# Optimization experiments

Hardware: AMD Instinct MI355X
Metric: run time of the kernel (lower is better)

Reference implementation:

```python
import jax, jax.numpy as jnp
import numpy as np

N, D, DOUT = 8192, 128, 128

def setup_inputs() -> dict:
    key = jax.random.key(0)
    k0, k1, k2, k3, k4 = jax.random.split(key, 5)
    return {
        "inputs": jnp.zeros((N, DOUT, 1, 2), jnp.float32),   # output buffer, scatter target
        "adj_pos": jax.random.uniform(k0, (N, N), jnp.float32),
        "adj_neg": jax.random.uniform(k1, (N, N), jnp.float32),
        "h0": jax.random.normal(k2, (N, D), jnp.float32),
        "WB0": jax.random.normal(k3, (DOUT, 2 * D), jnp.float32) * 0.05,
        "WU0": jax.random.normal(k4, (DOUT, 2 * D), jnp.float32) * 0.05,
        "start": 0,
        "end": N,
    }

def reference(inputs, adj_pos, adj_neg, h0, WB0, WU0, start, end):
    # self vectors for the row range [start, end)
    self_vec = h0[start:end]                                   # [n, D]

    def branch(adj, W):
        mask = adj[start:end]                                  # [n, N]
        # masked neighbor aggregation (dense adj matmul) + mean normalization
        agg = (mask @ h0) / jnp.sum(mask, axis=1, keepdims=True)  # [n, D]
        # concat(self-aggregate) -> small matmul (transpose_b=True) -> relu
        feat = jnp.concatenate([agg, self_vec], axis=1)        # [n, 2D]
        return jax.nn.relu(feat @ W.T)                         # [n, DOUT]

    # scatter-assign into the 4-D buffer, slot 0 = balanced, slot 1 = unbalanced
    inputs = inputs.at[start:end, :, 0, 0].set(branch(adj_pos, WB0))
    inputs = inputs.at[start:end, :, 0, 1].set(branch(adj_neg, WU0))
    return inputs
```

## Files before the change

kernel.cpp:

```cpp
#include <hip/hip_runtime.h>
#include <hip/hip_bf16.h>


typedef __bf16 bf16_t;
typedef __attribute__((ext_vector_type(8))) __bf16 bf16x8;
typedef __attribute__((ext_vector_type(4))) float f32x4;

#define KD    8192
#define DD    128
#define NROWS 8192
#define BK    32
#define NSTEP (KD / BK)
#define FLD   136

__device__ __forceinline__ bf16_t to_bf16(float x) { return (bf16_t)x; }

__device__ __forceinline__ bf16x8 cvt8(f32x4 a, f32x4 b) {
    bf16x8 r;
    r[0] = to_bf16(a[0]); r[1] = to_bf16(a[1]); r[2] = to_bf16(a[2]); r[3] = to_bf16(a[3]);
    r[4] = to_bf16(b[0]); r[5] = to_bf16(b[1]); r[6] = to_bf16(b[2]); r[7] = to_bf16(b[3]);
    return r;
}

__global__ void prep_h0T(const float* __restrict__ h0, bf16_t* __restrict__ h0T) {
    __shared__ bf16_t lt[128 * 72];
    const int tid = threadIdx.x;
    const int r0  = blockIdx.x * 64;
#pragma unroll
    for (int i = 0; i < 8; ++i) {
        const int e  = tid + i * 256;
        const int r  = e >> 5;
        const int c4 = e & 31;
        f32x4 v = *(const f32x4*)(h0 + (size_t)(r0 + r) * DD + c4 * 4);
        lt[(c4 * 4 + 0) * 72 + r] = to_bf16(v[0]);
        lt[(c4 * 4 + 1) * 72 + r] = to_bf16(v[1]);
        lt[(c4 * 4 + 2) * 72 + r] = to_bf16(v[2]);
        lt[(c4 * 4 + 3) * 72 + r] = to_bf16(v[3]);
    }
    __syncthreads();
    const int d = tid >> 1, half = tid & 1;
#pragma unroll
    for (int j = 0; j < 4; ++j) {
        bf16x8 v = *(const bf16x8*)(lt + d * 72 + half * 32 + j * 8);
        *(bf16x8*)(h0T + (size_t)d * KD + r0 + half * 32 + j * 8) = v;
    }
}

__global__ __launch_bounds__(256, 1)
void fused_gcn(const float* __restrict__ inputs0,
               const float* __restrict__ adj_pos,
               const float* __restrict__ adj_neg,
               const float* __restrict__ h0,
               const float* __restrict__ WB0,
               const float* __restrict__ WU0,
               const bf16_t* __restrict__ h0T,
               const int* __restrict__ startp,
               const int* __restrict__ endp,
               float* __restrict__ out) {
    __shared__ bf16_t feat[4][16 * FLD];

    const int tid  = threadIdx.x;
    const int wv   = tid >> 6;
    const int lane = tid & 63;
    const int l15  = lane & 15;
    const int quad = lane >> 4;
    const int br   = blockIdx.y;
    const int m0   = (blockIdx.x * 4 + wv) * 16;

    const float* __restrict__ adj  = br ? adj_neg : adj_pos;
    const float* __restrict__ Wmat = br ? WU0 : WB0;

    const float*  ap = adj + (size_t)(m0 + l15) * KD + quad * 8;
    const bf16_t* bp = h0T + (size_t)l15 * KD + quad * 8;

    f32x4 acc[8];
#pragma unroll
    for (int j = 0; j < 8; ++j) acc[j] = (f32x4){0.f, 0.f, 0.f, 0.f};
    float rsum = 0.f;

    f32x4 a0[2], a1[2];
    bf16x8 bfr[2][8];
#pragma unroll
    for (int p = 0; p < 2; ++p) {
        const float* a = ap + p * BK;
        a0[p] = *(const f32x4*)(a);
        a1[p] = *(const f32x4*)(a + 4);
#pragma unroll
        for (int j = 0; j < 8; ++j)
            bfr[p][j] = *(const bf16x8*)(bp + (size_t)j * 16 * KD + p * BK);
    }

#pragma unroll 2
    for (int kt = 0; kt < NSTEP; ++kt) {
        const int p = kt & 1;
        f32x4 va = a0[p], vb = a1[p];
        rsum += va[0] + va[1] + va[2] + va[3] + vb[0] + vb[1] + vb[2] + vb[3];
        bf16x8 afrag = cvt8(va, vb);
        if (kt + 2 < NSTEP) {
            const float* a = ap + (kt + 2) * BK;
            a0[p] = *(const f32x4*)(a);
            a1[p] = *(const f32x4*)(a + 4);
        }
#pragma unroll
        for (int j = 0; j < 8; ++j)
            acc[j] = __builtin_amdgcn_mfma_f32_16x16x32_bf16(afrag, bfr[p][j], acc[j], 0, 0, 0);
        if (kt + 2 < NSTEP) {
#pragma unroll
            for (int j = 0; j < 8; ++j)
                bfr[p][j] = *(const bf16x8*)(bp + (size_t)j * 16 * KD + (kt + 2) * BK);
        }
    }

    rsum += __shfl_xor(rsum, 16);
    rsum += __shfl_xor(rsum, 32);
    float inv_rs[4];
#pragma unroll
    for (int i = 0; i < 4; ++i)
        inv_rs[i] = 1.0f / __shfl(rsum, quad * 4 + i);

    bf16_t* fw = feat[wv];
#pragma unroll
    for (int j = 0; j < 8; ++j)
#pragma unroll
        for (int i = 0; i < 4; ++i)
            fw[(quad * 4 + i) * FLD + l15 + j * 16] = to_bf16(acc[j][i] * inv_rs[i]);

    __syncthreads();

    f32x4 o[8];
#pragma unroll
    for (int j = 0; j < 8; ++j) o[j] = (f32x4){0.f, 0.f, 0.f, 0.f};
#pragma unroll
    for (int ks = 0; ks < 8; ++ks) {
        bf16x8 af;
        if (ks < 4) {
            af = *(const bf16x8*)(fw + l15 * FLD + ks * 32 + quad * 8);
        } else {
            const float* hp = h0 + (size_t)(m0 + l15) * DD + (ks - 4) * 32 + quad * 8;
            af = cvt8(*(const f32x4*)(hp), *(const f32x4*)(hp + 4));
        }
#pragma unroll
        for (int j = 0; j < 8; ++j) {
            const float* wp = Wmat + (size_t)(j * 16 + l15) * 256 + ks * 32 + quad * 8;
            bf16x8 bf = cvt8(*(const f32x4*)(wp), *(const f32x4*)(wp + 4));
            o[j] = __builtin_amdgcn_mfma_f32_16x16x32_bf16(af, bf, o[j], 0, 0, 0);
        }
    }

    const int s = startp[0], e = endp[0];
#pragma unroll
    for (int j = 0; j < 8; ++j)
#pragma unroll
        for (int i = 0; i < 4; ++i) {
            const int grow = m0 + quad * 4 + i;
            const size_t idx = (size_t)grow * 256 + (size_t)(j * 16 + l15) * 2 + br;
            float v;
            if (grow >= s && grow < e) v = fmaxf(o[j][i], 0.f);
            else                       v = inputs0[idx];
            out[idx] = v;
        }
}

extern "C" void kernel_launch(void* const* d_in, const int* in_sizes, int n_in,
                              void* d_out, int out_size, void* d_ws, size_t ws_size,
                              hipStream_t stream) {
    const float* inputs0 = (const float*)d_in[0];
    const float* adj_pos = (const float*)d_in[1];
    const float* adj_neg = (const float*)d_in[2];
    const float* h0      = (const float*)d_in[3];
    const float* WB0     = (const float*)d_in[4];
    const float* WU0     = (const float*)d_in[5];
    const int*   startp  = (const int*)d_in[6];
    const int*   endp    = (const int*)d_in[7];
    float*       out     = (float*)d_out;

    const size_t need = (size_t)DD * KD * sizeof(bf16_t);
    bf16_t* h0T = (ws_size >= need) ? (bf16_t*)d_ws : (bf16_t*)d_in[0];

    prep_h0T<<<128, 256, 0, stream>>>(h0, h0T);
    dim3 grid(NROWS / 64, 2);
    fused_gcn<<<grid, 256, 0, stream>>>(inputs0, adj_pos, adj_neg, h0, WB0, WU0,
                                        h0T, startp, endp, out);
}
```

Measured before the change: 729.2 us.

## Deepen adjacency prefetch pipeline to eight stages with permuted K layout

Increases the register prefetch depth for adjacency rows from two to eight k-steps so more global loads are in flight per wave, targeting the latency-bound fp32 adjacency stream. The per-lane K mapping of the A fragment is changed (two 16-byte reads 16 floats apart), and the h0 transpose kernel permutes its output to match. Scheduling barriers pin the order of loads and MFMAs. This costs extra VGPRs and a restructured main loop with a peeled tail.

```diff
diff --git a/kernel.cpp b/kernel.cpp
--- a/kernel.cpp
+++ b/kernel.cpp
@@ -3,6 +3,7 @@
 
 
 typedef __bf16 bf16_t;
+typedef __attribute__((ext_vector_type(4))) __bf16 bf16x4;
 typedef __attribute__((ext_vector_type(8))) __bf16 bf16x8;
 typedef __attribute__((ext_vector_type(4))) float f32x4;
 
@@ -11,6 +12,7 @@
 #define NROWS 8192
 #define BK    32
 #define NSTEP (KD / BK)
+#define DEPTH 8
 #define FLD   136
 
 __device__ __forceinline__ bf16_t to_bf16(float x) { return (bf16_t)x; }
@@ -39,9 +41,14 @@
     }
     __syncthreads();
     const int d = tid >> 1, half = tid & 1;
+    const bf16_t* src = lt + d * 72 + half * 32;
 #pragma unroll
     for (int j = 0; j < 4; ++j) {
-        bf16x8 v = *(const bf16x8*)(lt + d * 72 + half * 32 + j * 8);
+        bf16x4 lo = *(const bf16x4*)(src + j * 4);
+        bf16x4 hi = *(const bf16x4*)(src + 16 + j * 4);
+        bf16x8 v;
+        v[0] = lo[0]; v[1] = lo[1]; v[2] = lo[2]; v[3] = lo[3];
+        v[4] = hi[0]; v[5] = hi[1]; v[6] = hi[2]; v[7] = hi[3];
         *(bf16x8*)(h0T + (size_t)d * KD + r0 + half * 32 + j * 8) = v;
     }
 }
@@ -70,44 +77,60 @@
     const float* __restrict__ adj  = br ? adj_neg : adj_pos;
     const float* __restrict__ Wmat = br ? WU0 : WB0;
 
-    const float*  ap = adj + (size_t)(m0 + l15) * KD + quad * 8;
-    const bf16_t* bp = h0T + (size_t)l15 * KD + quad * 8;
+    const float*  arow = adj + (size_t)(m0 + l15) * KD + quad * 4;
+    const bf16_t* bp   = h0T + (size_t)l15 * KD + quad * 8;
 
     f32x4 acc[8];
 #pragma unroll
     for (int j = 0; j < 8; ++j) acc[j] = (f32x4){0.f, 0.f, 0.f, 0.f};
     float rsum = 0.f;
 
-    f32x4 a0[2], a1[2];
+    f32x4 a0[DEPTH], a1[DEPTH];
     bf16x8 bfr[2][8];
 #pragma unroll
-    for (int p = 0; p < 2; ++p) {
-        const float* a = ap + p * BK;
-        a0[p] = *(const f32x4*)(a);
-        a1[p] = *(const f32x4*)(a + 4);
+    for (int p = 0; p < DEPTH; ++p) {
+        a0[p] = *(const f32x4*)(arow + p * BK);
+        a1[p] = *(const f32x4*)(arow + p * BK + 16);
+    }
+#pragma unroll
+    for (int p = 0; p < 2; ++p)
 #pragma unroll
         for (int j = 0; j < 8; ++j)
             bfr[p][j] = *(const bf16x8*)(bp + (size_t)j * 16 * KD + p * BK);
-    }
-
-#pragma unroll 2
-    for (int kt = 0; kt < NSTEP; ++kt) {
-        const int p = kt & 1;
-        f32x4 va = a0[p], vb = a1[p];
+
+    for (int kb = 0; kb < (NSTEP - DEPTH) / DEPTH; ++kb) {
+#pragma unroll
+        for (int i = 0; i < DEPTH; ++i) {
+            const int kt = kb * DEPTH + i;
+            f32x4 va = a0[i], vb = a1[i];
+            rsum += va[0] + va[1] + va[2] + va[3] + vb[0] + vb[1] + vb[2] + vb[3];
+            bf16x8 afrag = cvt8(va, vb);
+            a0[i] = *(const f32x4*)(arow + (kt + DEPTH) * BK);
+            a1[i] = *(const f32x4*)(arow + (kt + DEPTH) * BK + 16);
+            __builtin_amdgcn_sched_barrier(0);
+#pragma unroll
+            for (int j = 0; j < 8; ++j)
+                acc[j] = __builtin_amdgcn_mfma_f32_16x16x32_bf16(afrag, bfr[i & 1][j], acc[j], 0, 0, 0);
+            __builtin_amdgcn_sched_barrier(0);
+#pragma unroll
+            for (int j = 0; j < 8; ++j)
+                bfr[i & 1][j] = *(const bf16x8*)(bp + (size_t)j * 16 * KD + (kt + 2) * BK);
+        }
+    }
+
+#pragma unroll
+    for (int i = 0; i < DEPTH; ++i) {
+        const int kt = NSTEP - DEPTH + i;
+        f32x4 va = a0[i], vb = a1[i];
         rsum += va[0] + va[1] + va[2] + va[3] + vb[0] + vb[1] + vb[2] + vb[3];
         bf16x8 afrag = cvt8(va, vb);
+#pragma unroll
+        for (int j = 0; j < 8; ++j)
+            acc[j] = __builtin_amdgcn_mfma_f32_16x16x32_bf16(afrag, bfr[i & 1][j], acc[j], 0, 0, 0);
         if (kt + 2 < NSTEP) {
-            const float* a = ap + (kt + 2) * BK;
-            a0[p] = *(const f32x4*)(a);
-            a1[p] = *(const f32x4*)(a + 4);
-        }
-#pragma unroll
-        for (int j = 0; j < 8; ++j)
-            acc[j] = __builtin_amdgcn_mfma_f32_16x16x32_bf16(afrag, bfr[p][j], acc[j], 0, 0, 0);
-        if (kt + 2 < NSTEP) {
 #pragma unroll
             for (int j = 0; j < 8; ++j)
-                bfr[p][j] = *(const bf16x8*)(bp + (size_t)j * 16 * KD + (kt + 2) * BK);
+                bfr[i & 1][j] = *(const bf16x8*)(bp + (size_t)j * 16 * KD + (kt + 2) * BK);
         }
     }
 
```

Result: slower. 762.3 us (+4.5%).
